# Performance work log

Measured on AMD Instinct MI355X. Metric: run time of the kernel, lower is better.

## Reference

```python
import jax, jax.numpy as jnp
import numpy as np

IN_CAPS, IN_DIM, OUT_CAPS, OUT_DIM = 2048, 8, 32, 16
NUM_ROUTING = 3
EPS = 1e-9


def squash(s):
    # s: [..., out_dim]
    s2 = jnp.sum(s * s, axis=-1, keepdims=True)
    return (s2 / (1.0 + s2)) * (s / jnp.sqrt(s2 + EPS))


def setup_inputs() -> dict:
    key = jax.random.key(0)
    kx, kw = jax.random.split(key)
    x = jax.random.normal(kx, (64, IN_CAPS, IN_DIM), dtype=jnp.float32)
    W = jax.random.normal(kw, (1, IN_CAPS, OUT_CAPS, OUT_DIM, IN_DIM), dtype=jnp.float32) * 0.01
    return {"x": x, "W": W}


def reference(x, W):
    # u_hat[b,i,o,j] = sum_d W[0,i,o,j,d] * x[b,i,d]
    u_hat = jnp.einsum('iojd,bid->bioj', W[0], x)  # [B, in_caps, out_caps, out_dim]
    b_ij = jnp.zeros(u_hat.shape[:3], dtype=u_hat.dtype)  # [B, in_caps, out_caps]
    v_j = None
    for r in range(NUM_ROUTING):
        c_ij = jax.nn.softmax(b_ij, axis=2)[..., None]  # [B, in, out, 1]
        s_j = jnp.sum(c_ij * u_hat, axis=1)             # [B, out, out_dim]
        v_j = squash(s_j)
        if r < NUM_ROUTING - 1:
            b_ij = b_ij + jnp.einsum('bioj,boj->bio', u_hat, v_j)
    return v_j
```

## Files before the change

kernel.cpp:

```cpp
#include <hip/hip_runtime.h>
#include <math.h>


#define IC 2048
#define ID 8
#define OC 32
#define OD 16
#define B_N 64
#define S_ELEMS (B_N * OC * OD)
#define IB 16
#define ISTR (IC / IB)
#define BPB 16
#define BG (B_N / BPB)
#define ROWQ 65
#define NREG (8 * ROWQ)


template <int FIRST>
__launch_bounds__(256, 2)
__global__ void caps_pass(const float* __restrict__ Wg,
                          const float* __restrict__ xg,
                          const float* __restrict__ vs,
                          float* __restrict__ part)
{
    __shared__ float4 WA[2][NREG];
    __shared__ float4 WB[2][NREG];
    __shared__ float4 xs[2][BPB * 2];

    const int tid  = threadIdx.x;
    const int lane = tid & 63;
    const int w    = tid >> 6;
    const int o    = lane & 31;
    const int jh   = lane >> 5;
    const int c    = (o << 1) | jh;

    const int is   = blockIdx.x & (ISTR - 1);
    const int bg   = blockIdx.x >> 7;
    const int bblk = bg * BPB;
    const int bw   = bblk + w * 4;

    const float4* wq = (const float4*)Wg;

    auto put = [&](int parity, int Q, float4 v) {
        const int cw = Q >> 4;
        const int qq = Q & 15;
        float4* dst = (qq & 1) ? &WB[parity][(qq >> 1) * ROWQ + cw]
                               : &WA[parity][(qq >> 1) * ROWQ + cw];
        *dst = v;
    };

    float4 va[4], vb[4];
    if (!FIRST) {
#pragma unroll
        for (int n = 0; n < 4; ++n) {
            const float4* vp =
                (const float4*)(vs + (size_t)(bw + n) * (OC * OD) + o * OD + jh * 8);
            va[n] = vp[0];
            vb[n] = vp[1];
        }
    }

    float acc[4][8];
#pragma unroll
    for (int n = 0; n < 4; ++n)
#pragma unroll
        for (int jj = 0; jj < 8; ++jj) acc[n][jj] = 0.0f;

    {
        const int ig = is * IB;
        const size_t wb0 = (size_t)ig * 1024;
        float4 g0 = wq[wb0 + 0 * 256 + tid];
        float4 g1 = wq[wb0 + 1 * 256 + tid];
        float4 g2 = wq[wb0 + 2 * 256 + tid];
        float4 g3 = wq[wb0 + 3 * 256 + tid];
        float4 gx = {};
        if (tid < 32)
            gx = ((const float4*)xg)[((size_t)(bblk + (tid >> 1)) * IC + ig) * 2 + (tid & 1)];
        put(0, 0 * 256 + tid, g0);
        put(0, 1 * 256 + tid, g1);
        put(0, 2 * 256 + tid, g2);
        put(0, 3 * 256 + tid, g3);
        if (tid < 32) xs[0][tid] = gx;
    }

#pragma unroll 2
    for (int il = 0; il < IB; ++il) {
        const int p = il & 1;
        __syncthreads();

        float4 g0 = {}, g1 = {}, g2 = {}, g3 = {}, gx = {};
        const bool more = (il + 1 < IB);
        if (more) {
            const int ig = is * IB + il + 1;
            const size_t wb0 = (size_t)ig * 1024;
            g0 = wq[wb0 + 0 * 256 + tid];
            g1 = wq[wb0 + 1 * 256 + tid];
            g2 = wq[wb0 + 2 * 256 + tid];
            g3 = wq[wb0 + 3 * 256 + tid];
            if (tid < 32)
                gx = ((const float4*)xg)[((size_t)(bblk + (tid >> 1)) * IC + ig) * 2 + (tid & 1)];
        }

        float4 xa[4], xb[4];
#pragma unroll
        for (int n = 0; n < 4; ++n) {
            xa[n] = xs[p][(w * 4 + n) * 2];
            xb[n] = xs[p][(w * 4 + n) * 2 + 1];
        }

        float u[4][8];
#pragma unroll
        for (int jj = 0; jj < 8; ++jj) {
            const float4 wa = WA[p][jj * ROWQ + c];
            const float4 wbq = WB[p][jj * ROWQ + c];
#pragma unroll
            for (int n = 0; n < 4; ++n) {
                float t = wa.x * xa[n].x;
                t = fmaf(wa.y, xa[n].y, t);
                t = fmaf(wa.z, xa[n].z, t);
                t = fmaf(wa.w, xa[n].w, t);
                t = fmaf(wbq.x, xb[n].x, t);
                t = fmaf(wbq.y, xb[n].y, t);
                t = fmaf(wbq.z, xb[n].z, t);
                t = fmaf(wbq.w, xb[n].w, t);
                u[n][jj] = t;
            }
        }

#pragma unroll
        for (int n = 0; n < 4; ++n) {
            float cc;
            if (FIRST) {
                cc = 1.0f;
            } else {
                float bp = u[n][0] * va[n].x;
                bp = fmaf(u[n][1], va[n].y, bp);
                bp = fmaf(u[n][2], va[n].z, bp);
                bp = fmaf(u[n][3], va[n].w, bp);
                bp = fmaf(u[n][4], vb[n].x, bp);
                bp = fmaf(u[n][5], vb[n].y, bp);
                bp = fmaf(u[n][6], vb[n].z, bp);
                bp = fmaf(u[n][7], vb[n].w, bp);
                bp += __shfl_xor(bp, 32);
                const float e = __expf(bp);
                float se = e;
                se += __shfl_xor(se, 16);
                se += __shfl_xor(se, 8);
                se += __shfl_xor(se, 4);
                se += __shfl_xor(se, 2);
                se += __shfl_xor(se, 1);
                cc = e * __builtin_amdgcn_rcpf(se);
            }
#pragma unroll
            for (int jj = 0; jj < 8; ++jj)
                acc[n][jj] = fmaf(cc, u[n][jj], acc[n][jj]);
        }

        if (more) {
            put(p ^ 1, 0 * 256 + tid, g0);
            put(p ^ 1, 1 * 256 + tid, g1);
            put(p ^ 1, 2 * 256 + tid, g2);
            put(p ^ 1, 3 * 256 + tid, g3);
            if (tid < 32) xs[p ^ 1][tid] = gx;
        }
    }

    const float scale = FIRST ? (1.0f / 32.0f) : 1.0f;
#pragma unroll
    for (int n = 0; n < 4; ++n) {
        float* dst = part + (size_t)is * S_ELEMS + (size_t)(bw + n) * (OC * OD) + o * OD + jh * 8;
        float4 lo = {acc[n][0] * scale, acc[n][1] * scale, acc[n][2] * scale, acc[n][3] * scale};
        float4 hi = {acc[n][4] * scale, acc[n][5] * scale, acc[n][6] * scale, acc[n][7] * scale};
        ((float4*)dst)[0] = lo;
        ((float4*)dst)[1] = hi;
    }
}

template <int MODE>
__global__ void caps_reduce(const float* __restrict__ part,
                            float* __restrict__ vsum,
                            float* __restrict__ out)
{
    const int e = blockIdx.x * 256 + threadIdx.x;
    float s = 0.0f;
#pragma unroll 16
    for (int k = 0; k < ISTR; ++k)
        s += part[(size_t)k * S_ELEMS + e];
    float s2 = s * s;
    s2 += __shfl_xor(s2, 1);
    s2 += __shfl_xor(s2, 2);
    s2 += __shfl_xor(s2, 4);
    s2 += __shfl_xor(s2, 8);
    const float v = s * (s2 / ((1.0f + s2) * sqrtf(s2 + 1e-9f)));
    if (MODE == 0)      vsum[e] = v;
    else if (MODE == 1) vsum[e] += v;
    else                out[e] = v;
}

extern "C" void kernel_launch(void* const* d_in, const int* in_sizes, int n_in,
                              void* d_out, int out_size, void* d_ws, size_t ws_size,
                              hipStream_t stream)
{
    const float* x = (const float*)d_in[0];
    const float* W = (const float*)d_in[1];
    float* out = (float*)d_out;

    float* part = (float*)d_ws;
    float* vsum = part + (size_t)ISTR * S_ELEMS;

    const dim3 g(BG * ISTR);
    const dim3 b(256);
    const dim3 rg(S_ELEMS / 256);

    caps_pass<1><<<g, b, 0, stream>>>(W, x, nullptr, part);
    caps_reduce<0><<<rg, b, 0, stream>>>(part, vsum, out);
    caps_pass<0><<<g, b, 0, stream>>>(W, x, vsum, part);
    caps_reduce<1><<<rg, b, 0, stream>>>(part, vsum, out);
    caps_pass<0><<<g, b, 0, stream>>>(W, x, vsum, part);
    caps_reduce<2><<<rg, b, 0, stream>>>(part, vsum, out);
}
```

Before: 181.8 us.

## Use direct global-to-LDS loads with XOR swizzle, halve block, widen per-thread batch

The pass kernel now loads W straight into LDS with global_load_lds into an XOR-swizzled layout, removing the register staging and padded LDS scatter. It runs 128-thread blocks where each wave handles 8 batch rows and keeps W fragments in registers across them. The softmax sum over 32 lanes now uses DPP row ops plus one shuffle. The reduce kernel splits the 128-way partial sum across 4 waves and combines them in LDS. The risks are lower occupancy from the larger accumulator set and ordering hazards on the direct LDS loads.

```diff
diff --git a/kernel.cpp b/kernel.cpp
--- a/kernel.cpp
+++ b/kernel.cpp
@@ -12,189 +12,201 @@
 #define ISTR (IC / IB)
 #define BPB 16
 #define BG (B_N / BPB)
-#define ROWQ 65
-#define NREG (8 * ROWQ)
+
+__device__ __forceinline__ void gll16(const float4* g, float4* l)
+{
+    __builtin_amdgcn_global_load_lds(
+        (const __attribute__((address_space(1))) void*)g,
+        (__attribute__((address_space(3))) void*)l,
+        16, 0, 0);
+}
+
+template <int CTRL>
+__device__ __forceinline__ float dpp_add(float x)
+{
+    union { float f; int i; } a, b;
+    a.f = x;
+    b.i = __builtin_amdgcn_update_dpp(0, a.i, CTRL, 0xF, 0xF, true);
+    return x + b.f;
+}
 
 
 template <int FIRST>
-__launch_bounds__(256, 2)
+__launch_bounds__(128, 1)
 __global__ void caps_pass(const float* __restrict__ Wg,
                           const float* __restrict__ xg,
                           const float* __restrict__ vs,
                           float* __restrict__ part)
 {
-    __shared__ float4 WA[2][NREG];
-    __shared__ float4 WB[2][NREG];
-    __shared__ float4 xs[2][BPB * 2];
+    __shared__ float4 Wl[2][1024];
+    __shared__ float4 xsh[2][BPB * 2];
 
     const int tid  = threadIdx.x;
     const int lane = tid & 63;
     const int w    = tid >> 6;
     const int o    = lane & 31;
     const int jh   = lane >> 5;
-    const int c    = (o << 1) | jh;
 
     const int is   = blockIdx.x & (ISTR - 1);
     const int bg   = blockIdx.x >> 7;
     const int bblk = bg * BPB;
-    const int bw   = bblk + w * 4;
 
     const float4* wq = (const float4*)Wg;
 
-    auto put = [&](int parity, int Q, float4 v) {
-        const int cw = Q >> 4;
-        const int qq = Q & 15;
-        float4* dst = (qq & 1) ? &WB[parity][(qq >> 1) * ROWQ + cw]
-                               : &WA[parity][(qq >> 1) * ROWQ + cw];
-        *dst = v;
-    };
-
-    float4 va[4], vb[4];
+    float4 va[8], vb[8];
     if (!FIRST) {
 #pragma unroll
-        for (int n = 0; n < 4; ++n) {
-            const float4* vp =
-                (const float4*)(vs + (size_t)(bw + n) * (OC * OD) + o * OD + jh * 8);
-            va[n] = vp[0];
-            vb[n] = vp[1];
-        }
-    }
-
-    float acc[4][8];
-#pragma unroll
-    for (int n = 0; n < 4; ++n)
+        for (int n = 0; n < 8; ++n) {
+            const float* vp =
+                vs + (size_t)(bblk + w * 8 + n) * (OC * OD) + o * OD + jh * 8;
+            va[n] = ((const float4*)vp)[0];
+            vb[n] = ((const float4*)vp)[1];
+        }
+    }
+
+    float acc[8][8];
+#pragma unroll
+    for (int n = 0; n < 8; ++n)
 #pragma unroll
         for (int jj = 0; jj < 8; ++jj) acc[n][jj] = 0.0f;
 
     {
         const int ig = is * IB;
         const size_t wb0 = (size_t)ig * 1024;
-        float4 g0 = wq[wb0 + 0 * 256 + tid];
-        float4 g1 = wq[wb0 + 1 * 256 + tid];
-        float4 g2 = wq[wb0 + 2 * 256 + tid];
-        float4 g3 = wq[wb0 + 3 * 256 + tid];
-        float4 gx = {};
+#pragma unroll
+        for (int s = 0; s < 8; ++s) {
+            const int D = s * 128 + tid;
+            const int orow = D >> 5;
+            const int f = orow * 32 + ((D & 31) ^ orow);
+            gll16(wq + wb0 + f, &Wl[0][D]);
+        }
         if (tid < 32)
-            gx = ((const float4*)xg)[((size_t)(bblk + (tid >> 1)) * IC + ig) * 2 + (tid & 1)];
-        put(0, 0 * 256 + tid, g0);
-        put(0, 1 * 256 + tid, g1);
-        put(0, 2 * 256 + tid, g2);
-        put(0, 3 * 256 + tid, g3);
-        if (tid < 32) xs[0][tid] = gx;
-    }
-
-#pragma unroll 2
+            xsh[0][tid] = ((const float4*)xg)
+                [((size_t)(bblk + (tid >> 1)) * IC + ig) * 2 + (tid & 1)];
+    }
+
     for (int il = 0; il < IB; ++il) {
         const int p = il & 1;
         __syncthreads();
 
-        float4 g0 = {}, g1 = {}, g2 = {}, g3 = {}, gx = {};
+        float4 gx = {};
         const bool more = (il + 1 < IB);
         if (more) {
             const int ig = is * IB + il + 1;
             const size_t wb0 = (size_t)ig * 1024;
-            g0 = wq[wb0 + 0 * 256 + tid];
-            g1 = wq[wb0 + 1 * 256 + tid];
-            g2 = wq[wb0 + 2 * 256 + tid];
-            g3 = wq[wb0 + 3 * 256 + tid];
+#pragma unroll
+            for (int s = 0; s < 8; ++s) {
+                const int D = s * 128 + tid;
+                const int orow = D >> 5;
+                const int f = orow * 32 + ((D & 31) ^ orow);
+                gll16(wq + wb0 + f, &Wl[p ^ 1][D]);
+            }
             if (tid < 32)
-                gx = ((const float4*)xg)[((size_t)(bblk + (tid >> 1)) * IC + ig) * 2 + (tid & 1)];
-        }
-
-        float4 xa[4], xb[4];
-#pragma unroll
-        for (int n = 0; n < 4; ++n) {
-            xa[n] = xs[p][(w * 4 + n) * 2];
-            xb[n] = xs[p][(w * 4 + n) * 2 + 1];
-        }
-
-        float u[4][8];
+                gx = ((const float4*)xg)
+                    [((size_t)(bblk + (tid >> 1)) * IC + ig) * 2 + (tid & 1)];
+        }
+
+        float4 wA[8], wB[8];
+        const int row = o * 32;
 #pragma unroll
         for (int jj = 0; jj < 8; ++jj) {
-            const float4 wa = WA[p][jj * ROWQ + c];
-            const float4 wbq = WB[p][jj * ROWQ + c];
-#pragma unroll
-            for (int n = 0; n < 4; ++n) {
-                float t = wa.x * xa[n].x;
-                t = fmaf(wa.y, xa[n].y, t);
-                t = fmaf(wa.z, xa[n].z, t);
-                t = fmaf(wa.w, xa[n].w, t);
-                t = fmaf(wbq.x, xb[n].x, t);
-                t = fmaf(wbq.y, xb[n].y, t);
-                t = fmaf(wbq.z, xb[n].z, t);
-                t = fmaf(wbq.w, xb[n].w, t);
-                u[n][jj] = t;
+            const int ca = (jh * 16 + jj * 2) ^ o;
+            wA[jj] = Wl[p][row + ca];
+            wB[jj] = Wl[p][row + (ca ^ 1)];
+        }
+
+#pragma unroll
+        for (int n = 0; n < 8; ++n) {
+            const float4 xa = xsh[p][(w * 8 + n) * 2];
+            const float4 xb = xsh[p][(w * 8 + n) * 2 + 1];
+            float u[8];
+#pragma unroll
+            for (int jj = 0; jj < 8; ++jj) {
+                float t = wA[jj].x * xa.x;
+                t = fmaf(wA[jj].y, xa.y, t);
+                t = fmaf(wA[jj].z, xa.z, t);
+                t = fmaf(wA[jj].w, xa.w, t);
+                t = fmaf(wB[jj].x, xb.x, t);
+                t = fmaf(wB[jj].y, xb.y, t);
+                t = fmaf(wB[jj].z, xb.z, t);
+                t = fmaf(wB[jj].w, xb.w, t);
+                u[jj] = t;
             }
-        }
-
-#pragma unroll
-        for (int n = 0; n < 4; ++n) {
             float cc;
             if (FIRST) {
                 cc = 1.0f;
             } else {
-                float bp = u[n][0] * va[n].x;
-                bp = fmaf(u[n][1], va[n].y, bp);
-                bp = fmaf(u[n][2], va[n].z, bp);
-                bp = fmaf(u[n][3], va[n].w, bp);
-                bp = fmaf(u[n][4], vb[n].x, bp);
-                bp = fmaf(u[n][5], vb[n].y, bp);
-                bp = fmaf(u[n][6], vb[n].z, bp);
-                bp = fmaf(u[n][7], vb[n].w, bp);
+                float bp = u[0] * va[n].x;
+                bp = fmaf(u[1], va[n].y, bp);
+                bp = fmaf(u[2], va[n].z, bp);
+                bp = fmaf(u[3], va[n].w, bp);
+                bp = fmaf(u[4], vb[n].x, bp);
+                bp = fmaf(u[5], vb[n].y, bp);
+                bp = fmaf(u[6], vb[n].z, bp);
+                bp = fmaf(u[7], vb[n].w, bp);
                 bp += __shfl_xor(bp, 32);
                 const float e = __expf(bp);
-                float se = e;
-                se += __shfl_xor(se, 16);
-                se += __shfl_xor(se, 8);
-                se += __shfl_xor(se, 4);
-                se += __shfl_xor(se, 2);
-                se += __shfl_xor(se, 1);
+                float t = dpp_add<0xB1>(e);
+                t = dpp_add<0x4E>(t);
+                t = dpp_add<0x124>(t);
+                t = dpp_add<0x128>(t);
+                const float se = t + __shfl_xor(t, 16);
                 cc = e * __builtin_amdgcn_rcpf(se);
             }
 #pragma unroll
             for (int jj = 0; jj < 8; ++jj)
-                acc[n][jj] = fmaf(cc, u[n][jj], acc[n][jj]);
-        }
-
-        if (more) {
-            put(p ^ 1, 0 * 256 + tid, g0);
-            put(p ^ 1, 1 * 256 + tid, g1);
-            put(p ^ 1, 2 * 256 + tid, g2);
-            put(p ^ 1, 3 * 256 + tid, g3);
-            if (tid < 32) xs[p ^ 1][tid] = gx;
-        }
+                acc[n][jj] = fmaf(cc, u[jj], acc[n][jj]);
+        }
+
+        if (more && tid < 32) xsh[p ^ 1][tid] = gx;
     }
 
     const float scale = FIRST ? (1.0f / 32.0f) : 1.0f;
 #pragma unroll
-    for (int n = 0; n < 4; ++n) {
-        float* dst = part + (size_t)is * S_ELEMS + (size_t)(bw + n) * (OC * OD) + o * OD + jh * 8;
-        float4 lo = {acc[n][0] * scale, acc[n][1] * scale, acc[n][2] * scale, acc[n][3] * scale};
-        float4 hi = {acc[n][4] * scale, acc[n][5] * scale, acc[n][6] * scale, acc[n][7] * scale};
+    for (int n = 0; n < 8; ++n) {
+        float* dst = part + (size_t)is * S_ELEMS
+                   + (size_t)(bblk + w * 8 + n) * (OC * OD) + o * OD + jh * 8;
+        float4 lo = {acc[n][0] * scale, acc[n][1] * scale,
+                     acc[n][2] * scale, acc[n][3] * scale};
+        float4 hi = {acc[n][4] * scale, acc[n][5] * scale,
+                     acc[n][6] * scale, acc[n][7] * scale};
         ((float4*)dst)[0] = lo;
         ((float4*)dst)[1] = hi;
     }
 }
 
 template <int MODE>
+__launch_bounds__(256, 4)
 __global__ void caps_reduce(const float* __restrict__ part,
                             float* __restrict__ vsum,
                             float* __restrict__ out)
 {
-    const int e = blockIdx.x * 256 + threadIdx.x;
+    __shared__ float red[4][64];
+    const int tid  = threadIdx.x;
+    const int w    = tid >> 6;
+    const int lane = tid & 63;
+    const int e0   = blockIdx.x * 64;
+
     float s = 0.0f;
-#pragma unroll 16
-    for (int k = 0; k < ISTR; ++k)
-        s += part[(size_t)k * S_ELEMS + e];
-    float s2 = s * s;
-    s2 += __shfl_xor(s2, 1);
-    s2 += __shfl_xor(s2, 2);
-    s2 += __shfl_xor(s2, 4);
-    s2 += __shfl_xor(s2, 8);
-    const float v = s * (s2 / ((1.0f + s2) * sqrtf(s2 + 1e-9f)));
-    if (MODE == 0)      vsum[e] = v;
-    else if (MODE == 1) vsum[e] += v;
-    else                out[e] = v;
+#pragma unroll 8
+    for (int k = w; k < ISTR; k += 4)
+        s += part[(size_t)k * S_ELEMS + e0 + lane];
+    red[w][lane] = s;
+    __syncthreads();
+
+    if (tid < 64) {
+        const float t = red[0][tid] + red[1][tid] + red[2][tid] + red[3][tid];
+        float s2 = t * t;
+        s2 += __shfl_xor(s2, 1);
+        s2 += __shfl_xor(s2, 2);
+        s2 += __shfl_xor(s2, 4);
+        s2 += __shfl_xor(s2, 8);
+        const float v = t * (s2 / ((1.0f + s2) * sqrtf(s2 + 1e-9f)));
+        const int e = e0 + tid;
+        if (MODE == 0)      vsum[e] = v;
+        else if (MODE == 1) vsum[e] += v;
+        else                out[e] = v;
+    }
 }
 
 extern "C" void kernel_launch(void* const* d_in, const int* in_sizes, int n_in,
@@ -208,14 +220,15 @@
     float* part = (float*)d_ws;
     float* vsum = part + (size_t)ISTR * S_ELEMS;
 
-    const dim3 g(BG * ISTR);
-    const dim3 b(256);
-    const dim3 rg(S_ELEMS / 256);
-
-    caps_pass<1><<<g, b, 0, stream>>>(W, x, nullptr, part);
-    caps_reduce<0><<<rg, b, 0, stream>>>(part, vsum, out);
-    caps_pass<0><<<g, b, 0, stream>>>(W, x, vsum, part);
-    caps_reduce<1><<<rg, b, 0, stream>>>(part, vsum, out);
-    caps_pass<0><<<g, b, 0, stream>>>(W, x, vsum, part);
-    caps_reduce<2><<<rg, b, 0, stream>>>(part, vsum, out);
-}
+    const dim3 gP(BG * ISTR);
+    const dim3 bP(128);
+    const dim3 gR(S_ELEMS / 64);
+    const dim3 bR(256);
+
+    caps_pass<1><<<gP, bP, 0, stream>>>(W, x, nullptr, part);
+    caps_reduce<0><<<gR, bR, 0, stream>>>(part, vsum, out);
+    caps_pass<0><<<gP, bP, 0, stream>>>(W, x, vsum, part);
+    caps_reduce<1><<<gR, bR, 0, stream>>>(part, vsum, out);
+    caps_pass<0><<<gP, bP, 0, stream>>>(W, x, vsum, part);
+    caps_reduce<2><<<gR, bR, 0, stream>>>(part, vsum, out);
+}
```

Measured after the change: 204.5 us. +12.5%, slower.
